# Kernel tuning notes

Hardware: AMD Instinct MI355X
Metric: run time of the kernel (lower is better)

Reference implementation:

```python
import jax, jax.numpy as jnp
import numpy as np

N = 100000
E = 600000
D_IN = 128
D_OUT = 128


def setup_inputs() -> dict:
    key = jax.random.key(0)
    k1, k2, k3, k4 = jax.random.split(key, 4)
    H = jax.random.normal(k1, (N, D_IN), dtype=jnp.float32)
    edge_index = jax.random.randint(k2, (2, E), 0, N, dtype=jnp.int64)
    # torch Linear default init: U(-1/sqrt(in), 1/sqrt(in)); scale-equivalent randn ok for reference
    bound = 1.0 / np.sqrt(D_IN)
    W = jax.random.uniform(k3, (D_OUT, D_IN), minval=-bound, maxval=bound, dtype=jnp.float32)
    b = jax.random.uniform(k4, (D_OUT,), minval=-bound, maxval=bound, dtype=jnp.float32)
    return {"H": H, "edge_index": edge_index, "W": W, "b": b}


def reference(H, edge_index, W, b):
    n = H.shape[0]
    # add self loops (PyG add_self_loops appends [i, i] for every node)
    loops = jnp.arange(n, dtype=edge_index.dtype)
    row = jnp.concatenate([edge_index[0], loops])  # [E + N]
    col = jnp.concatenate([edge_index[1], loops])
    # degree of destination nodes (row), as in pyg.utils.degree(row, N)
    deg = jax.ops.segment_sum(jnp.ones_like(row, dtype=H.dtype), row, num_segments=n)
    deg_inv_sqrt = jnp.where(deg > 0, jax.lax.rsqrt(jnp.maximum(deg, 1.0)), 0.0)
    norm = deg_inv_sqrt[row] * deg_inv_sqrt[col]  # [E + N]
    # linear transform on nodes
    Hl = H @ W.T + b  # [N, D_OUT]
    # gather source features, scale, scatter-add to destinations
    msg = Hl[col] * norm[:, None]  # [E + N, D_OUT]
    out = jax.ops.segment_sum(msg, row, num_segments=n)
    return jax.nn.relu(out)
```

## Files before the change

### kernel.cpp

```cpp
#include <hip/hip_runtime.h>
#include <hip/hip_bf16.h>

#define N_NODES 100000
#define N_EDGES 600000
#define DIM 128
#define CAP 40

typedef __attribute__((ext_vector_type(8))) short short8;
typedef __attribute__((ext_vector_type(4))) float f32x4;
typedef __attribute__((ext_vector_type(4))) int i32x4;
typedef __attribute__((ext_vector_type(4))) unsigned u32x4;

static __device__ __forceinline__ short f2bf(float f) {
    return __builtin_bit_cast(short, __float2bfloat16(f));
}
static __device__ __forceinline__ unsigned pack2(float a, float b) {
    unsigned lo = (unsigned short)__builtin_bit_cast(short, __float2bfloat16(a));
    unsigned hi = (unsigned short)__builtin_bit_cast(short, __float2bfloat16(b));
    return lo | (hi << 16);
}
static __device__ __forceinline__ float bflo(unsigned u) {
    return __builtin_bit_cast(float, u << 16);
}
static __device__ __forceinline__ float bfhi(unsigned u) {
    return __builtin_bit_cast(float, u & 0xffff0000u);
}

__global__ __launch_bounds__(256) void fill_kernel(
    const int* __restrict__ erow, const int* __restrict__ ecol,
    int* __restrict__ cursor, int* __restrict__ bucket)
{
    int e = blockIdx.x * 256 + threadIdx.x;
    if (e < N_EDGES) {
        int r = __builtin_nontemporal_load(erow + e);
        int c = __builtin_nontemporal_load(ecol + e);
        if ((unsigned)r < (unsigned)N_NODES) {
            int pos = atomicAdd(&cursor[r], 1);
            if ((unsigned)pos < (unsigned)CAP)
                bucket[(size_t)r * CAP + pos] = c;
        }
    }
}

__global__ __launch_bounds__(256) void linear_mfma(
    const float* __restrict__ H, const float* __restrict__ W,
    const float* __restrict__ b, const int* __restrict__ cursor,
    __hip_bfloat16* __restrict__ Hl)
{
    __shared__ __hip_bfloat16 Wb[DIM][DIM + 8];

    const int t = threadIdx.x;
    const int wave = t >> 6;
    const int lane = t & 63;
    const int quad = lane >> 4;
    const int l16  = lane & 15;

    const int node0 = blockIdx.x * 128 + wave * 16 + l16;
    const int node1 = node0 + 64;
    const bool v0 = node0 < N_NODES;
    const bool v1 = node1 < N_NODES;

    f32x4 ha[4][2], hb[4][2];
    float dna = 0.f, dnb = 0.f;
    if (v0) {
        const f32x4* hp = (const f32x4*)(H + (size_t)node0 * DIM);
        #pragma unroll
        for (int ks = 0; ks < 4; ++ks) {
            ha[ks][0] = __builtin_nontemporal_load(hp + ks * 8 + quad * 2);
            ha[ks][1] = __builtin_nontemporal_load(hp + ks * 8 + quad * 2 + 1);
        }
        int d = cursor[node0];
        d = min(max(d, 0), CAP);
        dna = rsqrtf((float)d + 1.0f);
    } else {
        #pragma unroll
        for (int ks = 0; ks < 4; ++ks)
            ha[ks][0] = ha[ks][1] = (f32x4){0.f, 0.f, 0.f, 0.f};
    }
    if (v1) {
        const f32x4* hp = (const f32x4*)(H + (size_t)node1 * DIM);
        #pragma unroll
        for (int ks = 0; ks < 4; ++ks) {
            hb[ks][0] = __builtin_nontemporal_load(hp + ks * 8 + quad * 2);
            hb[ks][1] = __builtin_nontemporal_load(hp + ks * 8 + quad * 2 + 1);
        }
        int d = cursor[node1];
        d = min(max(d, 0), CAP);
        dnb = rsqrtf((float)d + 1.0f);
    } else {
        #pragma unroll
        for (int ks = 0; ks < 4; ++ks)
            hb[ks][0] = hb[ks][1] = (f32x4){0.f, 0.f, 0.f, 0.f};
    }

    for (int i = t; i < DIM * (DIM / 4); i += 256) {
        int row = i >> 5, c4 = i & 31;
        f32x4 w4 = ((const f32x4*)W)[i];
        __hip_bfloat16* dst = &Wb[row][c4 * 4];
        dst[0] = __float2bfloat16(w4.x);
        dst[1] = __float2bfloat16(w4.y);
        dst[2] = __float2bfloat16(w4.z);
        dst[3] = __float2bfloat16(w4.w);
    }
    __syncthreads();

    f32x4 acc[8];

    #pragma unroll
    for (int mt = 0; mt < 8; ++mt) acc[mt] = (f32x4){0.f, 0.f, 0.f, 0.f};
    #pragma unroll
    for (int ks = 0; ks < 4; ++ks) {
        const int k0 = ks * 32 + quad * 8;
        short8 hfr;
        hfr[0] = f2bf(ha[ks][0].x); hfr[1] = f2bf(ha[ks][0].y);
        hfr[2] = f2bf(ha[ks][0].z); hfr[3] = f2bf(ha[ks][0].w);
        hfr[4] = f2bf(ha[ks][1].x); hfr[5] = f2bf(ha[ks][1].y);
        hfr[6] = f2bf(ha[ks][1].z); hfr[7] = f2bf(ha[ks][1].w);
        #pragma unroll
        for (int mt = 0; mt < 8; ++mt) {
            short8 wfr = *(const short8*)&Wb[mt * 16 + l16][k0];
            acc[mt] = __builtin_amdgcn_mfma_f32_16x16x32_bf16(wfr, hfr, acc[mt], 0, 0, 0);
        }
    }
    if (v0) {
        #pragma unroll
        for (int mt = 0; mt < 8; ++mt) {
            f32x4 b4 = *(const f32x4*)(b + mt * 16 + quad * 4);
            uint2 pk;
            pk.x = pack2((acc[mt][0] + b4.x) * dna, (acc[mt][1] + b4.y) * dna);
            pk.y = pack2((acc[mt][2] + b4.z) * dna, (acc[mt][3] + b4.w) * dna);
            *(uint2*)(Hl + (size_t)node0 * DIM + mt * 16 + quad * 4) = pk;
        }
    }

    #pragma unroll
    for (int mt = 0; mt < 8; ++mt) acc[mt] = (f32x4){0.f, 0.f, 0.f, 0.f};
    #pragma unroll
    for (int ks = 0; ks < 4; ++ks) {
        const int k0 = ks * 32 + quad * 8;
        short8 hfr;
        hfr[0] = f2bf(hb[ks][0].x); hfr[1] = f2bf(hb[ks][0].y);
        hfr[2] = f2bf(hb[ks][0].z); hfr[3] = f2bf(hb[ks][0].w);
        hfr[4] = f2bf(hb[ks][1].x); hfr[5] = f2bf(hb[ks][1].y);
        hfr[6] = f2bf(hb[ks][1].z); hfr[7] = f2bf(hb[ks][1].w);
        #pragma unroll
        for (int mt = 0; mt < 8; ++mt) {
            short8 wfr = *(const short8*)&Wb[mt * 16 + l16][k0];
            acc[mt] = __builtin_amdgcn_mfma_f32_16x16x32_bf16(wfr, hfr, acc[mt], 0, 0, 0);
        }
    }
    if (v1) {
        #pragma unroll
        for (int mt = 0; mt < 8; ++mt) {
            f32x4 b4 = *(const f32x4*)(b + mt * 16 + quad * 4);
            uint2 pk;
            pk.x = pack2((acc[mt][0] + b4.x) * dnb, (acc[mt][1] + b4.y) * dnb);
            pk.y = pack2((acc[mt][2] + b4.z) * dnb, (acc[mt][3] + b4.w) * dnb);
            *(uint2*)(Hl + (size_t)node1 * DIM + mt * 16 + quad * 4) = pk;
        }
    }
}

static __device__ __forceinline__ void gather_one(
    int node, int d, i32x4 ia, i32x4 ib, u32x4 hs,
    const i32x4* __restrict__ bp, const u32x4* __restrict__ HlV,
    float* __restrict__ out, int l)
{
    d = min(max(d, 0), CAP);
    float dn = rsqrtf((float)d + 1.0f);

    float acc0 = bflo(hs.x), acc1 = bfhi(hs.x);
    float acc2 = bflo(hs.y), acc3 = bfhi(hs.y);
    float acc4 = bflo(hs.z), acc5 = bfhi(hs.z);
    float acc6 = bflo(hs.w), acc7 = bfhi(hs.w);

    int j = 0;
    for (;;) {
        int ids[8] = {ia.x, ia.y, ia.z, ia.w, ib.x, ib.y, ib.z, ib.w};
        u32x4 rows[8];
        float wgt[8];
        #pragma unroll
        for (int k = 0; k < 8; ++k) {
            unsigned idx = (unsigned)ids[k];
            idx = (idx < (unsigned)N_NODES) ? idx : 0u;
            wgt[k] = (j + k) < d ? 1.0f : 0.0f;
            rows[k] = HlV[idx * 16u + (unsigned)l];
        }
        bool more = __any((j + 8) < d);
        if (more) {
            int q = (j + 8) >> 2;
            ia = __builtin_nontemporal_load(bp + q);
            ib = __builtin_nontemporal_load(bp + q + 1);
        }
        #pragma unroll
        for (int k = 0; k < 8; ++k) {
            acc0 = fmaf(bflo(rows[k].x), wgt[k], acc0);
            acc1 = fmaf(bfhi(rows[k].x), wgt[k], acc1);
            acc2 = fmaf(bflo(rows[k].y), wgt[k], acc2);
            acc3 = fmaf(bfhi(rows[k].y), wgt[k], acc3);
            acc4 = fmaf(bflo(rows[k].z), wgt[k], acc4);
            acc5 = fmaf(bfhi(rows[k].z), wgt[k], acc5);
            acc6 = fmaf(bflo(rows[k].w), wgt[k], acc6);
            acc7 = fmaf(bfhi(rows[k].w), wgt[k], acc7);
        }
        if (!more) break;
        j += 8;
    }

    f32x4 o0, o1;
    o0.x = fmaxf(acc0 * dn, 0.f);
    o0.y = fmaxf(acc1 * dn, 0.f);
    o0.z = fmaxf(acc2 * dn, 0.f);
    o0.w = fmaxf(acc3 * dn, 0.f);
    o1.x = fmaxf(acc4 * dn, 0.f);
    o1.y = fmaxf(acc5 * dn, 0.f);
    o1.z = fmaxf(acc6 * dn, 0.f);
    o1.w = fmaxf(acc7 * dn, 0.f);
    float* op = out + (size_t)node * DIM + l * 8;
    __builtin_nontemporal_store(o0, (f32x4*)op);
    __builtin_nontemporal_store(o1, (f32x4*)(op + 4));
}

__global__ __launch_bounds__(128) void gather_kernel(
    const int* __restrict__ cursor, const int* __restrict__ bucket,
    const __hip_bfloat16* __restrict__ Hl, float* __restrict__ out)
{
    const int t = threadIdx.x;
    const int lane = t & 63;
    const int g = lane >> 4;
    const int l = lane & 15;
    const int base = blockIdx.x * 16 + ((t >> 6) << 3);
    const int nodeA = base + g;
    const int nodeB = base + 4 + g;

    const u32x4* __restrict__ HlV = (const u32x4*)Hl;

    const i32x4* bpA = (const i32x4*)(bucket + (size_t)nodeA * CAP);
    const i32x4* bpB = (const i32x4*)(bucket + (size_t)nodeB * CAP);
    i32x4 iaA = __builtin_nontemporal_load(bpA);
    i32x4 ibA = __builtin_nontemporal_load(bpA + 1);
    i32x4 iaB = __builtin_nontemporal_load(bpB);
    i32x4 ibB = __builtin_nontemporal_load(bpB + 1);
    u32x4 hsA = HlV[(unsigned)nodeA * 16u + (unsigned)l];
    u32x4 hsB = HlV[(unsigned)nodeB * 16u + (unsigned)l];
    int dA = cursor[nodeA];
    int dB = cursor[nodeB];

    gather_one(nodeA, dA, iaA, ibA, hsA, bpA, HlV, out, l);
    gather_one(nodeB, dB, iaB, ibB, hsB, bpB, HlV, out, l);
}

extern "C" void kernel_launch(void* const* d_in, const int* in_sizes, int n_in,
                              void* d_out, int out_size, void* d_ws, size_t ws_size,
                              hipStream_t stream) {
    const float* H  = (const float*)d_in[0];
    const int*   ei = (const int*)d_in[1];
    const float* W  = (const float*)d_in[2];
    const float* b  = (const float*)d_in[3];
    float* out = (float*)d_out;

    char* ws = (char*)d_ws;
    __hip_bfloat16* Hl = (__hip_bfloat16*)(ws);
    int* cursor = (int*)(ws + 25600000);
    int* bucket = (int*)(ws + 26000000);

    const int* erow = ei;
    const int* ecol = ei + N_EDGES;

    hipMemsetAsync(cursor, 0, N_NODES * sizeof(int), stream);
    fill_kernel<<<(N_EDGES + 255) / 256, 256, 0, stream>>>(erow, ecol, cursor, bucket);
    linear_mfma<<<(N_NODES + 127) / 128, 256, 0, stream>>>(H, W, b, cursor, Hl);
    gather_kernel<<<(N_NODES + 15) / 16, 128, 0, stream>>>(cursor, bucket, Hl, out);
}
```

Baseline: 197.1 us.

## Fuse edge bucketing into linear kernel and move source normalization to gather

Measured after the change: 202.9 us. 1.03x slower.

```diff
diff --git a/kernel.cpp b/kernel.cpp
--- a/kernel.cpp
+++ b/kernel.cpp
@@ -5,6 +5,7 @@
 #define N_EDGES 600000
 #define DIM 128
 #define CAP 40
+#define EPB 768
 
 typedef __attribute__((ext_vector_type(8))) short short8;
 typedef __attribute__((ext_vector_type(4))) float f32x4;
@@ -26,25 +27,11 @@
     return __builtin_bit_cast(float, u & 0xffff0000u);
 }
 
-__global__ __launch_bounds__(256) void fill_kernel(
+__global__ __launch_bounds__(256) void linear_fill(
+    const float* __restrict__ H, const float* __restrict__ W,
+    const float* __restrict__ b,
     const int* __restrict__ erow, const int* __restrict__ ecol,
-    int* __restrict__ cursor, int* __restrict__ bucket)
-{
-    int e = blockIdx.x * 256 + threadIdx.x;
-    if (e < N_EDGES) {
-        int r = __builtin_nontemporal_load(erow + e);
-        int c = __builtin_nontemporal_load(ecol + e);
-        if ((unsigned)r < (unsigned)N_NODES) {
-            int pos = atomicAdd(&cursor[r], 1);
-            if ((unsigned)pos < (unsigned)CAP)
-                bucket[(size_t)r * CAP + pos] = c;
-        }
-    }
-}
-
-__global__ __launch_bounds__(256) void linear_mfma(
-    const float* __restrict__ H, const float* __restrict__ W,
-    const float* __restrict__ b, const int* __restrict__ cursor,
+    int* __restrict__ cursor, int* __restrict__ bucket,
     __hip_bfloat16* __restrict__ Hl)
 {
     __shared__ __hip_bfloat16 Wb[DIM][DIM + 8];
@@ -61,7 +48,6 @@
     const bool v1 = node1 < N_NODES;
 
     f32x4 ha[4][2], hb[4][2];
-    float dna = 0.f, dnb = 0.f;
     if (v0) {
         const f32x4* hp = (const f32x4*)(H + (size_t)node0 * DIM);
         #pragma unroll
@@ -69,9 +55,6 @@
             ha[ks][0] = __builtin_nontemporal_load(hp + ks * 8 + quad * 2);
             ha[ks][1] = __builtin_nontemporal_load(hp + ks * 8 + quad * 2 + 1);
         }
-        int d = cursor[node0];
-        d = min(max(d, 0), CAP);
-        dna = rsqrtf((float)d + 1.0f);
     } else {
         #pragma unroll
         for (int ks = 0; ks < 4; ++ks)
@@ -84,13 +67,23 @@
             hb[ks][0] = __builtin_nontemporal_load(hp + ks * 8 + quad * 2);
             hb[ks][1] = __builtin_nontemporal_load(hp + ks * 8 + quad * 2 + 1);
         }
-        int d = cursor[node1];
-        d = min(max(d, 0), CAP);
-        dnb = rsqrtf((float)d + 1.0f);
     } else {
         #pragma unroll
         for (int ks = 0; ks < 4; ++ks)
             hb[ks][0] = hb[ks][1] = (f32x4){0.f, 0.f, 0.f, 0.f};
+    }
+
+    int er[3], ec[3];
+    {
+        const int ebase = blockIdx.x * EPB + t;
+        #pragma unroll
+        for (int i = 0; i < 3; ++i) {
+            int e = ebase + i * 256;
+            bool ve = e < N_EDGES;
+            er[i] = ve ? __builtin_nontemporal_load(erow + e) : -1;
+            ec[i] = ve ? __builtin_nontemporal_load(ecol + e) : 0;
+            asm volatile("" : "+v"(er[i]), "+v"(ec[i]));
+        }
     }
 
     for (int i = t; i < DIM * (DIM / 4); i += 256) {
@@ -127,8 +120,8 @@
         for (int mt = 0; mt < 8; ++mt) {
             f32x4 b4 = *(const f32x4*)(b + mt * 16 + quad * 4);
             uint2 pk;
-            pk.x = pack2((acc[mt][0] + b4.x) * dna, (acc[mt][1] + b4.y) * dna);
-            pk.y = pack2((acc[mt][2] + b4.z) * dna, (acc[mt][3] + b4.w) * dna);
+            pk.x = pack2(acc[mt][0] + b4.x, acc[mt][1] + b4.y);
+            pk.y = pack2(acc[mt][2] + b4.z, acc[mt][3] + b4.w);
             *(uint2*)(Hl + (size_t)node0 * DIM + mt * 16 + quad * 4) = pk;
         }
     }
@@ -154,9 +147,19 @@
         for (int mt = 0; mt < 8; ++mt) {
             f32x4 b4 = *(const f32x4*)(b + mt * 16 + quad * 4);
             uint2 pk;
-            pk.x = pack2((acc[mt][0] + b4.x) * dnb, (acc[mt][1] + b4.y) * dnb);
-            pk.y = pack2((acc[mt][2] + b4.z) * dnb, (acc[mt][3] + b4.w) * dnb);
+            pk.x = pack2(acc[mt][0] + b4.x, acc[mt][1] + b4.y);
+            pk.y = pack2(acc[mt][2] + b4.z, acc[mt][3] + b4.w);
             *(uint2*)(Hl + (size_t)node1 * DIM + mt * 16 + quad * 4) = pk;
+        }
+    }
+
+    #pragma unroll
+    for (int i = 0; i < 3; ++i) {
+        int r = er[i];
+        if ((unsigned)r < (unsigned)N_NODES) {
+            int pos = atomicAdd(&cursor[r], 1);
+            if ((unsigned)pos < (unsigned)CAP)
+                bucket[(size_t)r * CAP + pos] = ec[i];
         }
     }
 }
@@ -164,33 +167,39 @@
 static __device__ __forceinline__ void gather_one(
     int node, int d, i32x4 ia, i32x4 ib, u32x4 hs,
     const i32x4* __restrict__ bp, const u32x4* __restrict__ HlV,
-    float* __restrict__ out, int l)
+    const int* __restrict__ cursor, float* __restrict__ out, int l)
 {
     d = min(max(d, 0), CAP);
     float dn = rsqrtf((float)d + 1.0f);
 
-    float acc0 = bflo(hs.x), acc1 = bfhi(hs.x);
-    float acc2 = bflo(hs.y), acc3 = bfhi(hs.y);
-    float acc4 = bflo(hs.z), acc5 = bfhi(hs.z);
-    float acc6 = bflo(hs.w), acc7 = bfhi(hs.w);
+    float acc0 = bflo(hs.x) * dn, acc1 = bfhi(hs.x) * dn;
+    float acc2 = bflo(hs.y) * dn, acc3 = bfhi(hs.y) * dn;
+    float acc4 = bflo(hs.z) * dn, acc5 = bfhi(hs.z) * dn;
+    float acc6 = bflo(hs.w) * dn, acc7 = bfhi(hs.w) * dn;
 
     int j = 0;
     for (;;) {
         int ids[8] = {ia.x, ia.y, ia.z, ia.w, ib.x, ib.y, ib.z, ib.w};
         u32x4 rows[8];
+        int   degs[8];
         float wgt[8];
         #pragma unroll
         for (int k = 0; k < 8; ++k) {
             unsigned idx = (unsigned)ids[k];
             idx = (idx < (unsigned)N_NODES) ? idx : 0u;
-            wgt[k] = (j + k) < d ? 1.0f : 0.0f;
             rows[k] = HlV[idx * 16u + (unsigned)l];
+            degs[k] = cursor[idx];
         }
         bool more = __any((j + 8) < d);
         if (more) {
             int q = (j + 8) >> 2;
             ia = __builtin_nontemporal_load(bp + q);
             ib = __builtin_nontemporal_load(bp + q + 1);
+        }
+        #pragma unroll
+        for (int k = 0; k < 8; ++k) {
+            int dk = min(max(degs[k], 0), CAP);
+            wgt[k] = ((j + k) < d) ? rsqrtf((float)dk + 1.0f) : 0.0f;
         }
         #pragma unroll
         for (int k = 0; k < 8; ++k) {
@@ -246,8 +255,8 @@
     int dA = cursor[nodeA];
     int dB = cursor[nodeB];
 
-    gather_one(nodeA, dA, iaA, ibA, hsA, bpA, HlV, out, l);
-    gather_one(nodeB, dB, iaB, ibB, hsB, bpB, HlV, out, l);
+    gather_one(nodeA, dA, iaA, ibA, hsA, bpA, HlV, cursor, out, l);
+    gather_one(nodeB, dB, iaB, ibB, hsB, bpB, HlV, cursor, out, l);
 }
 
 extern "C" void kernel_launch(void* const* d_in, const int* in_sizes, int n_in,
@@ -268,7 +277,7 @@
     const int* ecol = ei + N_EDGES;
 
     hipMemsetAsync(cursor, 0, N_NODES * sizeof(int), stream);
-    fill_kernel<<<(N_EDGES + 255) / 256, 256, 0, stream>>>(erow, ecol, cursor, bucket);
-    linear_mfma<<<(N_NODES + 127) / 128, 256, 0, stream>>>(H, W, b, cursor, Hl);
+    linear_fill<<<(N_NODES + 127) / 128, 256, 0, stream>>>(H, W, b, erow, ecol,
+                                                           cursor, bucket, Hl);
     gather_kernel<<<(N_NODES + 15) / 16, 128, 0, stream>>>(cursor, bucket, Hl, out);
 }
```
